# Performance work log

Hardware: AMD Instinct MI355X
Metric: run time of the kernel (lower is better)

## Reference

```python
import jax, jax.numpy as jnp
import numpy as np

N_NODES = 100000
N_EDGES = 3200000
D_FEAT = 256
LEAKY_ALPHA = 0.2  # tf.nn.leaky_relu default


def setup_inputs() -> dict:
    key = jax.random.key(0)
    k1, k2, k3 = jax.random.split(key, 3)
    x = jax.random.normal(k1, (N_NODES, D_FEAT), dtype=jnp.float32)
    edge_index = jax.random.randint(k2, (2, N_EDGES), 0, N_NODES, dtype=jnp.int32)
    # Glorot-ish scale for the dense projection
    W = jax.random.normal(k3, (D_FEAT, D_FEAT), dtype=jnp.float32) * (1.0 / np.sqrt(D_FEAT))
    b = jnp.zeros((D_FEAT,), dtype=jnp.float32)
    return {"x": x, "edge_index": edge_index, "W": W, "b": b}


def reference(x, edge_index, W, b):
    # LightGCN symmetric normalization: A_hat = D^-1/2 A D^-1/2 (no self-loops)
    N = x.shape[0]
    row = edge_index[0]  # target nodes
    col = edge_index[1]  # source nodes
    ones = jnp.ones(row.shape[0], dtype=x.dtype)
    deg = jax.ops.segment_sum(ones, row, num_segments=N)  # [N]
    deg_safe = jnp.where(deg > 0, deg, 1.0)
    dinv_sqrt = jnp.where(deg > 0, jax.lax.rsqrt(deg_safe), 0.0)  # [N]
    w = dinv_sqrt[row] * dinv_sqrt[col]  # [E] normalized edge weights
    # SpMM: h[i] = sum_{(i,j) in E} w_ij * x[j]
    h = jax.ops.segment_sum(w[:, None] * x[col], row, num_segments=N)  # [N, d]
    # Dense projection + leaky_relu (edge_drop_rate=0.0 / inference -> no dropout)
    h = h @ W + b
    return jnp.where(h >= 0, h, LEAKY_ALPHA * h)
```

## Files before the change

### kernel.cpp

```cpp
#include <hip/hip_runtime.h>
#include <hip/hip_bf16.h>

#define D 256
#define CH 8192

typedef __attribute__((ext_vector_type(8))) short bf16x8;
typedef __attribute__((ext_vector_type(4))) float f32x4;

static __device__ __forceinline__ unsigned int f2bf(float f) {
  __hip_bfloat16 b = __float2bfloat16(f);
  return (unsigned int)*reinterpret_cast<unsigned short*>(&b);
}
static __device__ __forceinline__ float u2f(unsigned int u) {
  return __uint_as_float(u);
}

static __device__ __forceinline__ void acc8w(float* acc, uint4 v, float wt) {
  acc[0] += wt * u2f(v.x << 16);
  acc[1] += wt * u2f(v.x & 0xffff0000u);
  acc[2] += wt * u2f(v.y << 16);
  acc[3] += wt * u2f(v.y & 0xffff0000u);
  acc[4] += wt * u2f(v.z << 16);
  acc[5] += wt * u2f(v.z & 0xffff0000u);
  acc[6] += wt * u2f(v.w << 16);
  acc[7] += wt * u2f(v.w & 0xffff0000u);
}


__global__ __launch_bounds__(256) void fused_prep_kernel(
    const int* __restrict__ row, const float* __restrict__ x, const float* __restrict__ W,
    uint4* __restrict__ xb0, uint4* __restrict__ xb1, __hip_bfloat16* __restrict__ Wt,
    int* __restrict__ counts, int E, int NB, int nblk, int total8, int convb) {
  __shared__ int hist[2048];
  int bid = blockIdx.x, tid = threadIdx.x;
  if (bid < nblk) {
    for (int t = tid; t < NB; t += 256) hist[t] = 0;
    __syncthreads();
    int e0 = bid * CH, e1 = min(E, e0 + CH);
    for (int e = e0 + tid; e < e1; e += 256) atomicAdd(&hist[row[e] >> 6], 1);
    __syncthreads();
    for (int t = tid; t < NB; t += 256) counts[(size_t)bid * NB + t] = hist[t];
  } else if (bid < nblk + convb) {
    int idx = (bid - nblk) * 256 + tid;
    if (idx < total8) {
      int j = idx >> 5, k8 = idx & 31;
      const float4* x4 = reinterpret_cast<const float4*>(x);
      float4 a = x4[(size_t)idx * 2], bb = x4[(size_t)idx * 2 + 1];
      uint4 o;
      o.x = f2bf(a.x) | (f2bf(a.y) << 16);
      o.y = f2bf(a.z) | (f2bf(a.w) << 16);
      o.z = f2bf(bb.x) | (f2bf(bb.y) << 16);
      o.w = f2bf(bb.z) | (f2bf(bb.w) << 16);
      uint4* dst = (k8 < 16) ? xb0 : xb1;
      dst[(size_t)j * 16 + (k8 & 15)] = o;
    }
  } else {
    int n = bid - nblk - convb;
    Wt[n * D + tid] = __float2bfloat16(W[tid * D + n]);
  }
}

__global__ void colscan_kernel(int* counts, int* total, int NB, int nblk) {
  int t = blockIdx.x * 256 + threadIdx.x;
  if (t >= NB) return;
  int run = 0;
#pragma unroll 4
  for (int blk = 0; blk < nblk; ++blk) {
    size_t idx = (size_t)blk * NB + t;
    int c = counts[idx];
    counts[idx] = run;
    run += c;
  }
  total[t] = run;
}

__global__ void bucket_scan_kernel(const int* __restrict__ total, int* __restrict__ bucket_base,
                                   int NB) {
  __shared__ int a[2048], b2[2048];
  int t = threadIdx.x;
  for (int k = 0; k < 2; ++k) {
    int i = t + k * 1024;
    a[i] = (i < NB) ? total[i] : 0;
  }
  __syncthreads();
  int* cur = a;
  int* nxt = b2;
  for (int off = 1; off < 2048; off <<= 1) {
    for (int k = 0; k < 2; ++k) {
      int i = t + k * 1024;
      int v = cur[i];
      if (i >= off) v += cur[i - off];
      nxt[i] = v;
    }
    __syncthreads();
    int* tmp = cur; cur = nxt; nxt = tmp;
  }
  if (t == 0) bucket_base[0] = 0;
  for (int k = 0; k < 2; ++k) {
    int i = t + k * 1024;
    if (i < NB) bucket_base[i + 1] = cur[i];
  }
}

__global__ __launch_bounds__(256) void scatter_kernel(
    const int* __restrict__ row, const int* __restrict__ col, const int* __restrict__ counts,
    const int* __restrict__ bucket_base, unsigned int* __restrict__ sorted, int E, int NB) {
  __shared__ int base[2048];
  __shared__ int cur[2048];
  int bid = blockIdx.x, tid = threadIdx.x;
  for (int t = tid; t < NB; t += 256) {
    base[t] = bucket_base[t] + counts[(size_t)bid * NB + t];
    cur[t] = 0;
  }
  __syncthreads();
  int e0 = bid * CH, e1 = min(E, e0 + CH);
  for (int e = e0 + tid; e < e1; e += 256) {
    int r = row[e], c = col[e];
    int b = r >> 6;
    int p = base[b] + atomicAdd(&cur[b], 1);
    sorted[p] = ((unsigned int)(r & 63) << 17) | (unsigned int)c;
  }
}

__global__ __launch_bounds__(256) void bucket_csr_kernel(
    const unsigned int* __restrict__ sorted, const int* __restrict__ bucket_base,
    int* __restrict__ offsets, float* __restrict__ dinv, int* __restrict__ csr_col,
    int N, int E, int NB, int ncb) {
  __shared__ int cnt[1024];
  int b = blockIdx.x, tid = threadIdx.x;
  int lo = bucket_base[b], hi = bucket_base[b + 1];
  int slots = 64 * ncb;
  for (int t = tid; t < slots; t += 256) cnt[t] = 0;
  __syncthreads();
  for (int e = lo + tid; e < hi; e += 256) {
    unsigned int v = sorted[e];
    atomicAdd(&cnt[(v >> 17) * ncb + ((v & 0x1FFFFu) >> 13)], 1);
  }
  __syncthreads();
  if (tid == 0) {
    int run = 0;
    for (int i2 = 0; i2 < slots; ++i2) {
      int t2 = cnt[i2];
      cnt[i2] = run;
      run += t2;
    }
  }
  __syncthreads();
  if (tid < 64) {
    int gr = b * 64 + tid;
    if (gr < N) {
      int start = cnt[tid * ncb];
      int nxt = (tid == 63) ? (hi - lo) : cnt[(tid + 1) * ncb];
      int dg = nxt - start;
      offsets[gr] = lo + start;
      dinv[gr] = (dg > 0) ? rsqrtf((float)dg) : 0.f;
    }
  }
  if (b == NB - 1 && tid == 0) offsets[N] = E;
  __syncthreads();
  for (int e = lo + tid; e < hi; e += 256) {
    unsigned int v = sorted[e];
    int p = lo + atomicAdd(&cnt[(v >> 17) * ncb + ((v & 0x1FFFFu) >> 13)], 1);
    csr_col[p] = (int)(v & 0x1FFFFu);
  }
}

__global__ __launch_bounds__(256) void spmm_half_kernel(
    const int* __restrict__ offsets, const int* __restrict__ csr_col,
    const float* __restrict__ dinv, const uint4* __restrict__ xb,
    uint4* __restrict__ h, int N, int hoff) {
  int wave = threadIdx.x >> 6;
  int lane = threadIdx.x & 63;
  int i = blockIdx.x * 4 + wave;
  if (i >= N) return;
  int g = lane >> 4;
  int l = lane & 15;
  int beg = offsets[i], end = offsets[i + 1];

  float acc[8];
#pragma unroll
  for (int j = 0; j < 8; ++j) acc[j] = 0.f;

  int e = beg + g;
  for (; e + 12 < end; e += 16) {
    int c0 = csr_col[e], c1 = csr_col[e + 4], c2 = csr_col[e + 8], c3 = csr_col[e + 12];
    float w0 = dinv[c0], w1 = dinv[c1], w2 = dinv[c2], w3 = dinv[c3];
    uint4 v0 = xb[(size_t)c0 * 16 + l];
    uint4 v1 = xb[(size_t)c1 * 16 + l];
    uint4 v2 = xb[(size_t)c2 * 16 + l];
    uint4 v3 = xb[(size_t)c3 * 16 + l];
    acc8w(acc, v0, w0);
    acc8w(acc, v1, w1);
    acc8w(acc, v2, w2);
    acc8w(acc, v3, w3);
  }
  for (; e < end; e += 4) {
    int c = csr_col[e];
    float w = dinv[c];
    uint4 v = xb[(size_t)c * 16 + l];
    acc8w(acc, v, w);
  }

#pragma unroll
  for (int j = 0; j < 8; ++j) {
    acc[j] += __shfl(acc[j], lane ^ 16, 64);
    acc[j] += __shfl(acc[j], lane ^ 32, 64);
  }

  if (g == 0) {
    float di = dinv[i];
    uint4 o;
    o.x = f2bf(acc[0] * di) | (f2bf(acc[1] * di) << 16);
    o.y = f2bf(acc[2] * di) | (f2bf(acc[3] * di) << 16);
    o.z = f2bf(acc[4] * di) | (f2bf(acc[5] * di) << 16);
    o.w = f2bf(acc[6] * di) | (f2bf(acc[7] * di) << 16);
    h[(size_t)i * 32 + hoff + l] = o;
  }
}

__global__ void deg_rank_kernel(const int* __restrict__ row, int* __restrict__ deg,
                                unsigned short* __restrict__ rank, int E) {
  int e = blockIdx.x * blockDim.x + threadIdx.x;
  if (e < E) rank[e] = (unsigned short)atomicAdd(&deg[row[e]], 1);
}
__global__ void scan1(const int* __restrict__ deg, int* __restrict__ offsets,
                      int* __restrict__ partials, int n) {
  __shared__ int tmp[256];
  int i = blockIdx.x * 256 + threadIdx.x;
  int v = (i < n) ? deg[i] : 0;
  tmp[threadIdx.x] = v;
  __syncthreads();
  for (int off = 1; off < 256; off <<= 1) {
    int t = (threadIdx.x >= off) ? tmp[threadIdx.x - off] : 0;
    __syncthreads();
    tmp[threadIdx.x] += t;
    __syncthreads();
  }
  if (i < n) offsets[i] = tmp[threadIdx.x] - v;
  if (threadIdx.x == 255) partials[blockIdx.x] = tmp[255];
}
__global__ void scan2(int* __restrict__ partials, int nb) {
  __shared__ int tmp[512];
  int tid = threadIdx.x;
  int v = (tid < nb) ? partials[tid] : 0;
  tmp[tid] = v;
  __syncthreads();
  for (int off = 1; off < 512; off <<= 1) {
    int t = (tid >= off) ? tmp[tid - off] : 0;
    __syncthreads();
    tmp[tid] += t;
    __syncthreads();
  }
  if (tid < nb) partials[tid] = tmp[tid] - v;
}
__global__ void scan3(int* __restrict__ offsets, const int* __restrict__ partials,
                      const int* __restrict__ deg, float* __restrict__ dinv, int n, int E) {
  int i = blockIdx.x * 256 + threadIdx.x;
  if (i < n) {
    offsets[i] += partials[blockIdx.x];
    int d = deg[i];
    dinv[i] = (d > 0) ? rsqrtf((float)d) : 0.0f;
    if (i == 0) offsets[n] = E;
  }
}
__global__ void fill_kernel(const int* __restrict__ row, const int* __restrict__ col,
                            const int* __restrict__ offsets, const unsigned short* __restrict__ rank,
                            int* __restrict__ csr_col, int E) {
  int e = blockIdx.x * blockDim.x + threadIdx.x;
  if (e < E) {
    int pos = offsets[row[e]] + (int)rank[e];
    csr_col[pos] = col[e];
  }
}
__global__ void wt_kernel(const float* __restrict__ W, __hip_bfloat16* __restrict__ Wt) {
  int n = blockIdx.x, k = threadIdx.x;
  Wt[n * D + k] = __float2bfloat16(W[k * D + n]);
}
__global__ __launch_bounds__(256) void spmm_f32_kernel(
    const int* __restrict__ offsets, const int* __restrict__ csr_col,
    const float* __restrict__ dinv, const float* __restrict__ x,
    unsigned short* __restrict__ h, int N) {
  int wave = threadIdx.x >> 6;
  int lane = threadIdx.x & 63;
  int i = blockIdx.x * 4 + wave;
  if (i >= N) return;
  int beg = offsets[i], end = offsets[i + 1];
  float di = dinv[i];
  const float4* x4 = reinterpret_cast<const float4*>(x);
  float4 acc = make_float4(0.f, 0.f, 0.f, 0.f);
  for (int e = beg; e < end; ++e) {
    int c = csr_col[e];
    float w = di * dinv[c];
    float4 v = x4[(size_t)c * 64 + lane];
    acc.x += w * v.x; acc.y += w * v.y; acc.z += w * v.z; acc.w += w * v.w;
  }
  ushort4 o;
  o.x = (unsigned short)f2bf(acc.x);
  o.y = (unsigned short)f2bf(acc.y);
  o.z = (unsigned short)f2bf(acc.z);
  o.w = (unsigned short)f2bf(acc.w);
  *reinterpret_cast<ushort4*>(h + (size_t)i * D + lane * 4) = o;
}

__global__ __launch_bounds__(256, 2) void gemm_kernel(
    const __hip_bfloat16* __restrict__ h, const __hip_bfloat16* __restrict__ Wt,
    const float* __restrict__ bias, float* __restrict__ out, int M, int ntiles) {
  const int tid = threadIdx.x;
  const int wave = tid >> 6;
  const int lane = tid & 63;
  const int ncol = lane & 15;
  const int kgrp = (lane >> 4) * 8;
  const int rgrp = (lane >> 4) * 4;
  const int col0 = wave * 64;

  const short* hp = reinterpret_cast<const short*>(h);
  const short* wtp = reinterpret_cast<const short*>(Wt);

  bf16x8 breg[4][8];
#pragma unroll
  for (int nt = 0; nt < 4; ++nt)
#pragma unroll
    for (int kk = 0; kk < 8; ++kk)
      breg[nt][kk] =
          *reinterpret_cast<const bf16x8*>(wtp + (size_t)(col0 + nt * 16 + ncol) * D + kk * 32 + kgrp);

  float bv[4];
#pragma unroll
  for (int nt = 0; nt < 4; ++nt) bv[nt] = bias[col0 + nt * 16 + ncol];

  const int stride = gridDim.x;
  int t = blockIdx.x;
  if (t >= ntiles) return;

  bf16x8 a[8];
  {
    int arow = t * 16 + (lane & 15);
    int arow_c = (arow < M) ? arow : 0;
#pragma unroll
    for (int kk = 0; kk < 8; ++kk)
      a[kk] = *reinterpret_cast<const bf16x8*>(hp + (size_t)arow_c * D + kk * 32 + kgrp);
  }

  for (; t < ntiles; t += stride) {
    int tn = t + stride;
    bf16x8 an[8];
    if (tn < ntiles) {
      int arow = tn * 16 + (lane & 15);
      int arow_c = (arow < M) ? arow : 0;
#pragma unroll
      for (int kk = 0; kk < 8; ++kk)
        an[kk] = *reinterpret_cast<const bf16x8*>(hp + (size_t)arow_c * D + kk * 32 + kgrp);
    }

    f32x4 acc[4];
#pragma unroll
    for (int nt = 0; nt < 4; ++nt) acc[nt] = (f32x4){0.f, 0.f, 0.f, 0.f};
#pragma unroll
    for (int nt = 0; nt < 4; ++nt)
#pragma unroll
      for (int kk = 0; kk < 8; ++kk)
        acc[nt] = __builtin_amdgcn_mfma_f32_16x16x32_bf16(a[kk], breg[nt][kk], acc[nt], 0, 0, 0);

    int row0 = t * 16;
#pragma unroll
    for (int nt = 0; nt < 4; ++nt) {
      int col = col0 + nt * 16 + ncol;
#pragma unroll
      for (int r = 0; r < 4; ++r) {
        int row = row0 + rgrp + r;
        if (row < M) {
          float v = acc[nt][r] + bv[nt];
          out[(size_t)row * D + col] = (v >= 0.f) ? v : 0.2f * v;
        }
      }
    }

#pragma unroll
    for (int kk = 0; kk < 8; ++kk) a[kk] = an[kk];
  }
}

extern "C" void kernel_launch(void* const* d_in, const int* in_sizes, int n_in,
                              void* d_out, int out_size, void* d_ws, size_t ws_size,
                              hipStream_t stream) {
  const float* x = (const float*)d_in[0];
  const int* ei = (const int*)d_in[1];
  const float* W = (const float*)d_in[2];
  const float* b = (const float*)d_in[3];
  float* out = (float*)d_out;

  const int N = in_sizes[0] / D;
  const int E = in_sizes[1] / 2;
  const int* row = ei;
  const int* col = ei + E;

  char* ws = (char*)d_ws;
  size_t off = 0;
  auto alloc = [&](size_t bytes) -> void* {
    void* p = ws + off;
    off += (bytes + 255) & ~(size_t)255;
    return p;
  };
  auto align256 = [](size_t v) { return (v + 255) & ~(size_t)255; };

  int* offsets = (int*)alloc((size_t)(N + 1) * 4);
  float* dinv = (float*)alloc((size_t)N * 4);
  int* csr_col = (int*)alloc((size_t)E * 4);
  char* hreg = (char*)alloc((size_t)N * D * 2);
  __hip_bfloat16* Wt = (__hip_bfloat16*)alloc((size_t)D * D * 2);
  size_t tail_off = off;

  const int NB = (N + 63) >> 6;
  const int ncb = (N + 8191) >> 13;
  const int nblk = (E + CH - 1) / CH;
  const int total8 = N * D / 8;
  const int convb = (total8 + 255) / 256;

  size_t s_sorted = 0;
  size_t s_counts = s_sorted + align256((size_t)E * 4);
  size_t s_base = s_counts + align256((size_t)nblk * NB * 4);
  size_t s_total = s_base + align256((size_t)(NB + 1) * 4);
  size_t h_need = s_total + (size_t)NB * 4;

  size_t fast_need = tail_off + align256((size_t)N * D * 2);
  bool use_fast = (N <= 131072) && (NB <= 2048) && (ncb <= 16) &&
                  (h_need <= (size_t)N * D * 2) && (fast_need <= ws_size);

  unsigned short* h = (unsigned short*)hreg;

  if (use_fast) {
    unsigned int* sorted = (unsigned int*)(hreg + s_sorted);
    int* counts = (int*)(hreg + s_counts);
    int* bucket_base = (int*)(hreg + s_base);
    int* total = (int*)(hreg + s_total);
    uint4* xb0 = (uint4*)(ws + tail_off);
    uint4* xb1 = xb0 + (size_t)N * 16;

    fused_prep_kernel<<<nblk + convb + D, 256, 0, stream>>>(
        row, x, W, xb0, xb1, Wt, counts, E, NB, nblk, total8, convb);
    colscan_kernel<<<(NB + 255) / 256, 256, 0, stream>>>(counts, total, NB, nblk);
    bucket_scan_kernel<<<1, 1024, 0, stream>>>(total, bucket_base, NB);
    scatter_kernel<<<nblk, 256, 0, stream>>>(row, col, counts, bucket_base, sorted, E, NB);
    bucket_csr_kernel<<<NB, 256, 0, stream>>>(sorted, bucket_base, offsets, dinv, csr_col,
                                              N, E, NB, ncb);
    spmm_half_kernel<<<(N + 3) / 4, 256, 0, stream>>>(offsets, csr_col, dinv, xb0, (uint4*)h, N, 0);
    spmm_half_kernel<<<(N + 3) / 4, 256, 0, stream>>>(offsets, csr_col, dinv, xb1, (uint4*)h, N, 16);
  } else {
    size_t foff = tail_off;
    int* deg = (int*)(ws + foff); foff += align256((size_t)N * 4);
    int* partials = (int*)(ws + foff); foff += align256(512 * 4);
    unsigned short* rank = (unsigned short*)(ws + foff); foff += align256((size_t)E * 2);
    (void)hipMemsetAsync(deg, 0, (size_t)N * 4, stream);
    const int eb = (E + 255) / 256;
    const int nb = (N + 255) / 256;
    deg_rank_kernel<<<eb, 256, 0, stream>>>(row, deg, rank, E);
    scan1<<<nb, 256, 0, stream>>>(deg, offsets, partials, N);
    scan2<<<1, 512, 0, stream>>>(partials, nb);
    scan3<<<nb, 256, 0, stream>>>(offsets, partials, deg, dinv, N, E);
    fill_kernel<<<eb, 256, 0, stream>>>(row, col, offsets, rank, csr_col, E);
    wt_kernel<<<D, D, 0, stream>>>(W, Wt);
    spmm_f32_kernel<<<(N + 3) / 4, 256, 0, stream>>>(offsets, csr_col, dinv, x, h, N);
  }
  const int ntiles = (N + 15) / 16;
  int gB = ntiles < 512 ? ntiles : 512;
  gemm_kernel<<<gB, 256, 0, stream>>>((const __hip_bfloat16*)h, Wt, b, out, N, ntiles);
}
```

Before: 445.1 us.

## Coarsen radix buckets to 1024 rows and parallelize bucket scans

The first-level bucket sort now groups 1024 rows per bucket (98 buckets) instead of 64 (1563 buckets). This shrinks the per-block histogram and counts matrix and makes its layout bucket-major, so the column scan becomes a per-bucket parallel block scan. The second-level bucket_csr kernel runs with 512 threads and a large LDS counter array (1024 rows × ncb), using a parallel scan instead of a single-thread serial one. The cost is far fewer, heavier blocks in bucket_csr with high LDS use, which limits occupancy, and a tighter fast-path eligibility condition.

```diff
diff --git a/kernel.cpp b/kernel.cpp
--- a/kernel.cpp
+++ b/kernel.cpp
@@ -3,6 +3,7 @@
 
 #define D 256
 #define CH 8192
+#define MAXNCB 15
 
 typedef __attribute__((ext_vector_type(8))) short bf16x8;
 typedef __attribute__((ext_vector_type(4))) float f32x4;
@@ -30,16 +31,16 @@
 __global__ __launch_bounds__(256) void fused_prep_kernel(
     const int* __restrict__ row, const float* __restrict__ x, const float* __restrict__ W,
     uint4* __restrict__ xb0, uint4* __restrict__ xb1, __hip_bfloat16* __restrict__ Wt,
-    int* __restrict__ counts, int E, int NB, int nblk, int total8, int convb) {
-  __shared__ int hist[2048];
+    int* __restrict__ counts, int E, int NCBK, int nblk, int total8, int convb) {
+  __shared__ int hist[128];
   int bid = blockIdx.x, tid = threadIdx.x;
   if (bid < nblk) {
-    for (int t = tid; t < NB; t += 256) hist[t] = 0;
+    if (tid < 128) hist[tid] = 0;
     __syncthreads();
     int e0 = bid * CH, e1 = min(E, e0 + CH);
-    for (int e = e0 + tid; e < e1; e += 256) atomicAdd(&hist[row[e] >> 6], 1);
-    __syncthreads();
-    for (int t = tid; t < NB; t += 256) counts[(size_t)bid * NB + t] = hist[t];
+    for (int e = e0 + tid; e < e1; e += 256) atomicAdd(&hist[row[e] >> 10], 1);
+    __syncthreads();
+    for (int t = tid; t < NCBK; t += 256) counts[(size_t)t * nblk + bid] = hist[t];
   } else if (bid < nblk + convb) {
     int idx = (bid - nblk) * 256 + tid;
     if (idx < total8) {
@@ -60,34 +61,23 @@
   }
 }
 
-__global__ void colscan_kernel(int* counts, int* total, int NB, int nblk) {
-  int t = blockIdx.x * 256 + threadIdx.x;
-  if (t >= NB) return;
-  int run = 0;
-#pragma unroll 4
-  for (int blk = 0; blk < nblk; ++blk) {
-    size_t idx = (size_t)blk * NB + t;
-    int c = counts[idx];
-    counts[idx] = run;
-    run += c;
-  }
-  total[t] = run;
-}
-
-__global__ void bucket_scan_kernel(const int* __restrict__ total, int* __restrict__ bucket_base,
-                                   int NB) {
-  __shared__ int a[2048], b2[2048];
-  int t = threadIdx.x;
+__global__ __launch_bounds__(256) void colscan_kernel(int* __restrict__ counts,
+                                                      int* __restrict__ total, int nblk) {
+  __shared__ int a[512], bb[512];
+  int t = blockIdx.x, tid = threadIdx.x;
+  int* base = counts + (size_t)t * nblk;
+  int v0[2];
   for (int k = 0; k < 2; ++k) {
-    int i = t + k * 1024;
-    a[i] = (i < NB) ? total[i] : 0;
+    int i = tid + k * 256;
+    v0[k] = (i < nblk) ? base[i] : 0;
+    a[i] = v0[k];
   }
   __syncthreads();
   int* cur = a;
-  int* nxt = b2;
-  for (int off = 1; off < 2048; off <<= 1) {
+  int* nxt = bb;
+  for (int off = 1; off < 512; off <<= 1) {
     for (int k = 0; k < 2; ++k) {
-      int i = t + k * 1024;
+      int i = tid + k * 256;
       int v = cur[i];
       if (i >= off) v += cur[i - off];
       nxt[i] = v;
@@ -95,70 +85,112 @@
     __syncthreads();
     int* tmp = cur; cur = nxt; nxt = tmp;
   }
+  for (int k = 0; k < 2; ++k) {
+    int i = tid + k * 256;
+    if (i < nblk) {
+      base[i] = cur[i] - v0[k];
+      if (i == nblk - 1) total[t] = cur[i];
+    }
+  }
+}
+
+__global__ void bucket_scan_kernel(const int* __restrict__ total, int* __restrict__ bucket_base,
+                                   int NCBK) {
+  __shared__ int a[256], bb[256];
+  int t = threadIdx.x;
+  a[t] = (t < NCBK) ? total[t] : 0;
+  __syncthreads();
+  int* cur = a;
+  int* nxt = bb;
+  for (int off = 1; off < 256; off <<= 1) {
+    int v = cur[t];
+    if (t >= off) v += cur[t - off];
+    nxt[t] = v;
+    __syncthreads();
+    int* tmp = cur; cur = nxt; nxt = tmp;
+  }
   if (t == 0) bucket_base[0] = 0;
-  for (int k = 0; k < 2; ++k) {
-    int i = t + k * 1024;
-    if (i < NB) bucket_base[i + 1] = cur[i];
-  }
+  if (t < NCBK) bucket_base[t + 1] = cur[t];
 }
 
 __global__ __launch_bounds__(256) void scatter_kernel(
     const int* __restrict__ row, const int* __restrict__ col, const int* __restrict__ counts,
-    const int* __restrict__ bucket_base, unsigned int* __restrict__ sorted, int E, int NB) {
-  __shared__ int base[2048];
-  __shared__ int cur[2048];
+    const int* __restrict__ bucket_base, unsigned int* __restrict__ sorted, int E, int NCBK,
+    int nblk) {
+  __shared__ int base[128];
+  __shared__ int cur[128];
   int bid = blockIdx.x, tid = threadIdx.x;
-  for (int t = tid; t < NB; t += 256) {
-    base[t] = bucket_base[t] + counts[(size_t)bid * NB + t];
+  for (int t = tid; t < NCBK; t += 256) {
+    base[t] = bucket_base[t] + counts[(size_t)t * nblk + bid];
     cur[t] = 0;
   }
   __syncthreads();
   int e0 = bid * CH, e1 = min(E, e0 + CH);
   for (int e = e0 + tid; e < e1; e += 256) {
     int r = row[e], c = col[e];
-    int b = r >> 6;
+    int b = r >> 10;
     int p = base[b] + atomicAdd(&cur[b], 1);
-    sorted[p] = ((unsigned int)(r & 63) << 17) | (unsigned int)c;
-  }
-}
-
-__global__ __launch_bounds__(256) void bucket_csr_kernel(
+    sorted[p] = ((unsigned int)(r & 1023) << 17) | (unsigned int)c;
+  }
+}
+
+__global__ __launch_bounds__(512) void bucket_csr_kernel(
     const unsigned int* __restrict__ sorted, const int* __restrict__ bucket_base,
     int* __restrict__ offsets, float* __restrict__ dinv, int* __restrict__ csr_col,
-    int N, int E, int NB, int ncb) {
-  __shared__ int cnt[1024];
+    int N, int E, int NCBK, int ncb) {
+  __shared__ int cnt[1024 * MAXNCB];
+  __shared__ int auxa[512], auxb[512];
   int b = blockIdx.x, tid = threadIdx.x;
   int lo = bucket_base[b], hi = bucket_base[b + 1];
-  int slots = 64 * ncb;
-  for (int t = tid; t < slots; t += 256) cnt[t] = 0;
-  __syncthreads();
-  for (int e = lo + tid; e < hi; e += 256) {
+  int slots = 1024 * ncb;
+  for (int t = tid; t < slots; t += 512) cnt[t] = 0;
+  __syncthreads();
+  for (int e = lo + tid; e < hi; e += 512) {
     unsigned int v = sorted[e];
     atomicAdd(&cnt[(v >> 17) * ncb + ((v & 0x1FFFFu) >> 13)], 1);
   }
   __syncthreads();
-  if (tid == 0) {
-    int run = 0;
-    for (int i2 = 0; i2 < slots; ++i2) {
-      int t2 = cnt[i2];
-      cnt[i2] = run;
-      run += t2;
-    }
-  }
-  __syncthreads();
-  if (tid < 64) {
-    int gr = b * 64 + tid;
+  int per = (slots + 511) / 512;
+  int i0 = tid * per;
+  int run = 0;
+  for (int k = 0; k < per; ++k) {
+    int i = i0 + k;
+    if (i < slots) {
+      int c = cnt[i];
+      cnt[i] = run;
+      run += c;
+    }
+  }
+  auxa[tid] = run;
+  __syncthreads();
+  int* cur = auxa;
+  int* nxt = auxb;
+  for (int off = 1; off < 512; off <<= 1) {
+    int v = cur[tid];
+    if (tid >= off) v += cur[tid - off];
+    nxt[tid] = v;
+    __syncthreads();
+    int* tmp = cur; cur = nxt; nxt = tmp;
+  }
+  int add = (tid > 0) ? cur[tid - 1] : 0;
+  for (int k = 0; k < per; ++k) {
+    int i = i0 + k;
+    if (i < slots) cnt[i] += add;
+  }
+  __syncthreads();
+  for (int nl = tid; nl < 1024; nl += 512) {
+    int gr = b * 1024 + nl;
     if (gr < N) {
-      int start = cnt[tid * ncb];
-      int nxt = (tid == 63) ? (hi - lo) : cnt[(tid + 1) * ncb];
-      int dg = nxt - start;
+      int start = cnt[nl * ncb];
+      int nxt_s = (nl == 1023) ? (hi - lo) : cnt[(nl + 1) * ncb];
+      int dg = nxt_s - start;
       offsets[gr] = lo + start;
       dinv[gr] = (dg > 0) ? rsqrtf((float)dg) : 0.f;
     }
   }
-  if (b == NB - 1 && tid == 0) offsets[N] = E;
-  __syncthreads();
-  for (int e = lo + tid; e < hi; e += 256) {
+  if (b == NCBK - 1 && tid == 0) offsets[N] = E;
+  __syncthreads();
+  for (int e = lo + tid; e < hi; e += 512) {
     unsigned int v = sorted[e];
     int p = lo + atomicAdd(&cnt[(v >> 17) * ncb + ((v & 0x1FFFFu) >> 13)], 1);
     csr_col[p] = (int)(v & 0x1FFFFu);
@@ -223,8 +255,8 @@
   int e = blockIdx.x * blockDim.x + threadIdx.x;
   if (e < E) rank[e] = (unsigned short)atomicAdd(&deg[row[e]], 1);
 }
-__global__ void scan1(const int* __restrict__ deg, int* __restrict__ offsets,
-                      int* __restrict__ partials, int n) {
+__global__ void fscan1(const int* __restrict__ deg, int* __restrict__ offsets,
+                       int* __restrict__ partials, int n) {
   __shared__ int tmp[256];
   int i = blockIdx.x * 256 + threadIdx.x;
   int v = (i < n) ? deg[i] : 0;
@@ -239,7 +271,7 @@
   if (i < n) offsets[i] = tmp[threadIdx.x] - v;
   if (threadIdx.x == 255) partials[blockIdx.x] = tmp[255];
 }
-__global__ void scan2(int* __restrict__ partials, int nb) {
+__global__ void fscan2(int* __restrict__ partials, int nb) {
   __shared__ int tmp[512];
   int tid = threadIdx.x;
   int v = (tid < nb) ? partials[tid] : 0;
@@ -253,8 +285,8 @@
   }
   if (tid < nb) partials[tid] = tmp[tid] - v;
 }
-__global__ void scan3(int* __restrict__ offsets, const int* __restrict__ partials,
-                      const int* __restrict__ deg, float* __restrict__ dinv, int n, int E) {
+__global__ void fscan3(int* __restrict__ offsets, const int* __restrict__ partials,
+                       const int* __restrict__ deg, float* __restrict__ dinv, int n, int E) {
   int i = blockIdx.x * 256 + threadIdx.x;
   if (i < n) {
     offsets[i] += partials[blockIdx.x];
@@ -410,7 +442,7 @@
   __hip_bfloat16* Wt = (__hip_bfloat16*)alloc((size_t)D * D * 2);
   size_t tail_off = off;
 
-  const int NB = (N + 63) >> 6;
+  const int NCBK = (N + 1023) >> 10;
   const int ncb = (N + 8191) >> 13;
   const int nblk = (E + CH - 1) / CH;
   const int total8 = N * D / 8;
@@ -418,12 +450,12 @@
 
   size_t s_sorted = 0;
   size_t s_counts = s_sorted + align256((size_t)E * 4);
-  size_t s_base = s_counts + align256((size_t)nblk * NB * 4);
-  size_t s_total = s_base + align256((size_t)(NB + 1) * 4);
-  size_t h_need = s_total + (size_t)NB * 4;
+  size_t s_base = s_counts + align256((size_t)NCBK * nblk * 4);
+  size_t s_total = s_base + align256((size_t)(NCBK + 1) * 4);
+  size_t h_need = s_total + (size_t)NCBK * 4;
 
   size_t fast_need = tail_off + align256((size_t)N * D * 2);
-  bool use_fast = (N <= 131072) && (NB <= 2048) && (ncb <= 16) &&
+  bool use_fast = (N <= 122880) && (NCBK <= 128) && (ncb <= MAXNCB) && (nblk <= 512) &&
                   (h_need <= (size_t)N * D * 2) && (fast_need <= ws_size);
 
   unsigned short* h = (unsigned short*)hreg;
@@ -437,12 +469,12 @@
     uint4* xb1 = xb0 + (size_t)N * 16;
 
     fused_prep_kernel<<<nblk + convb + D, 256, 0, stream>>>(
-        row, x, W, xb0, xb1, Wt, counts, E, NB, nblk, total8, convb);
-    colscan_kernel<<<(NB + 255) / 256, 256, 0, stream>>>(counts, total, NB, nblk);
-    bucket_scan_kernel<<<1, 1024, 0, stream>>>(total, bucket_base, NB);
-    scatter_kernel<<<nblk, 256, 0, stream>>>(row, col, counts, bucket_base, sorted, E, NB);
-    bucket_csr_kernel<<<NB, 256, 0, stream>>>(sorted, bucket_base, offsets, dinv, csr_col,
-                                              N, E, NB, ncb);
+        row, x, W, xb0, xb1, Wt, counts, E, NCBK, nblk, total8, convb);
+    colscan_kernel<<<NCBK, 256, 0, stream>>>(counts, total, nblk);
+    bucket_scan_kernel<<<1, 256, 0, stream>>>(total, bucket_base, NCBK);
+    scatter_kernel<<<nblk, 256, 0, stream>>>(row, col, counts, bucket_base, sorted, E, NCBK, nblk);
+    bucket_csr_kernel<<<NCBK, 512, 0, stream>>>(sorted, bucket_base, offsets, dinv, csr_col,
+                                                N, E, NCBK, ncb);
     spmm_half_kernel<<<(N + 3) / 4, 256, 0, stream>>>(offsets, csr_col, dinv, xb0, (uint4*)h, N, 0);
     spmm_half_kernel<<<(N + 3) / 4, 256, 0, stream>>>(offsets, csr_col, dinv, xb1, (uint4*)h, N, 16);
   } else {
@@ -454,9 +486,9 @@
     const int eb = (E + 255) / 256;
     const int nb = (N + 255) / 256;
     deg_rank_kernel<<<eb, 256, 0, stream>>>(row, deg, rank, E);
-    scan1<<<nb, 256, 0, stream>>>(deg, offsets, partials, N);
-    scan2<<<1, 512, 0, stream>>>(partials, nb);
-    scan3<<<nb, 256, 0, stream>>>(offsets, partials, deg, dinv, N, E);
+    fscan1<<<nb, 256, 0, stream>>>(deg, offsets, partials, N);
+    fscan2<<<1, 512, 0, stream>>>(partials, nb);
+    fscan3<<<nb, 256, 0, stream>>>(offsets, partials, deg, dinv, N, E);
     fill_kernel<<<eb, 256, 0, stream>>>(row, col, offsets, rank, csr_col, E);
     wt_kernel<<<D, D, 0, stream>>>(W, Wt);
     spmm_f32_kernel<<<(N + 3) / 4, 256, 0, stream>>>(offsets, csr_col, dinv, x, h, N);
```

After: 383.2 us. 13.9% less time.
